# Performance work log

Hardware: AMD Instinct MI355X
Metric: run time of the kernel (lower is better)

The kernel has to match this reference:

```python
import jax, jax.numpy as jnp
import numpy as np

B, T, C = 16, 512, 768
MULT = 4
D_IN = C * MULT          # 3072
HIDDEN = 1024
N_DATES = 16
STACK_SIZE, STACK_STRIDE = 4, 2
MAX_F = 512
N_MASK_TYPES = 5
N_SESSIONS = 4
SCALE = HIDDEN ** 0.5


def setup_inputs() -> dict:
    key = jax.random.key(0)
    ks = jax.random.split(key, 12)
    inp = {
        "spikes": jax.random.normal(ks[0], (B, T, C), dtype=jnp.float32),
        "spikes_mask": jnp.ones((B, T), dtype=jnp.int64),
        "spikes_timestamp": jax.random.randint(ks[1], (B, T), 0, 255).astype(jnp.int64),
        "date_idx": jax.random.randint(ks[2], (B,), 0, N_DATES).astype(jnp.int64),
        "mask_idx": 1,
        "session_idx": 3,
        # params
        "W_embed": jax.random.normal(ks[3], (N_DATES, D_IN, C), dtype=jnp.float32) * 0.02,
        "b_embed": jax.random.normal(ks[4], (N_DATES, D_IN), dtype=jnp.float32) * 0.02,
        "W_stack": jax.random.normal(ks[5], (HIDDEN, D_IN * STACK_SIZE), dtype=jnp.float32) * 0.02,
        "b_stack": jax.random.normal(ks[6], (HIDDEN,), dtype=jnp.float32) * 0.02,
        "pos_table": jax.random.normal(ks[7], (MAX_F, HIDDEN), dtype=jnp.float32) * 0.02,
        "prompt_table": jax.random.normal(ks[8], (N_MASK_TYPES, HIDDEN), dtype=jnp.float32) * 0.02,
        "session_table": jax.random.normal(ks[9], (N_SESSIONS, HIDDEN), dtype=jnp.float32) * 0.02,
    }
    return inp


def reference(spikes, spikes_mask, spikes_timestamp, date_idx, mask_idx, session_idx,
              W_embed, b_embed, W_stack, b_stack, pos_table, prompt_table, session_table):
    Bb = spikes.shape[0]
    # adapt branch: per-sample expert Linear, done as one gather + batched GEMM
    W = W_embed[date_idx]                      # [B, D_IN, C]
    b = b_embed[date_idx]                      # [B, D_IN]
    x = jnp.einsum('btc,bdc->btd', spikes, W) + b[:, None, :]   # [B, T, D_IN]
    x = jax.nn.gelu(x, approximate=False) * SCALE
    # unfold-based stacking: sliding windows over time
    L = (T - STACK_SIZE) // STACK_STRIDE + 1   # 255
    starts = jnp.arange(L) * STACK_STRIDE
    widx = starts[:, None] + jnp.arange(STACK_SIZE)             # [L, size]
    win = x[:, widx, :]                                         # [B, L, size, D_IN]
    stacked = win.reshape(Bb, L, STACK_SIZE * D_IN)
    x = stacked @ W_stack.T + b_stack                           # [B, L, HIDDEN]
    ts = spikes_timestamp[:, :L]
    mask = jnp.prod(spikes_mask[:, widx], axis=-1)              # [B, L]
    # positional embedding
    x = x + pos_table[ts]
    # prompt token
    x = jnp.concatenate(
        [jnp.broadcast_to(prompt_table[mask_idx][None, None, :], (Bb, 1, HIDDEN)), x], axis=1)
    mask = jnp.pad(mask, ((0, 0), (1, 0)), constant_values=1)
    ts = jnp.concatenate([jnp.zeros((Bb, 1), ts.dtype), ts + 1], axis=1)
    # session token
    x = jnp.concatenate(
        [jnp.broadcast_to(session_table[session_idx][None, None, :], (Bb, 1, HIDDEN)), x], axis=1)
    mask = jnp.pad(mask, ((0, 0), (1, 0)), constant_values=1)
    ts = jnp.concatenate([jnp.zeros((Bb, 1), ts.dtype), ts + 1], axis=1)
    # dropout is identity in eval
    return x, mask, ts
```

## Files before the change

### kernel.cpp

```cpp
#include <hip/hip_runtime.h>
#include <hip/hip_bf16.h>

#define BATCH   16
#define TT      512
#define CC      768
#define D_IN    3072
#define HIDDEN  1024
#define LL      255
#define OUTROWS 257
#define KSTACK  12288

typedef float f32x4 __attribute__((ext_vector_type(4)));
typedef __bf16 bf16x8 __attribute__((ext_vector_type(8)));
typedef unsigned short u16;

__device__ __forceinline__ u16 f2bf(float f) {
    unsigned u = __builtin_bit_cast(unsigned, f);
    u = (u + 0x7FFFu + ((u >> 16) & 1u)) >> 16;
    return (u16)u;
}

__device__ __forceinline__ bf16x8 lds_read8(const u16* p) {
    return __builtin_bit_cast(bf16x8, *(const uint4*)p);
}

__device__ __forceinline__ void gload16(const u16* g, u16* l) {
    __builtin_amdgcn_global_load_lds(
        (const __attribute__((address_space(1))) void*)g,
        (__attribute__((address_space(3))) void*)l, 16, 0, 0);
}

__global__ __launch_bounds__(256) void cvt_wstack(const float* __restrict__ W, u16* __restrict__ out) {
    size_t i = ((size_t)blockIdx.x * 256 + threadIdx.x) * 4;
    size_t stride = (size_t)gridDim.x * 256 * 4;
    for (; i < (size_t)HIDDEN * KSTACK; i += stride) {
        float4 v = *(const float4*)(W + i);
        ushort4 o = make_ushort4(f2bf(v.x), f2bf(v.y), f2bf(v.z), f2bf(v.w));
        *(ushort4*)(out + i) = o;
    }
}

__global__ __launch_bounds__(256) void gemm1(const float* __restrict__ spikes,
                                             const float* __restrict__ W_embed,
                                             const float* __restrict__ b_embed,
                                             const int* __restrict__ date_idx,
                                             u16* __restrict__ x1) {
    const int m0 = blockIdx.x * 128;
    const int n0 = blockIdx.y * 128;
    const int bb = blockIdx.z;
    const int date = date_idx[bb];
    const float* A  = spikes  + (size_t)bb  * TT * CC;
    const float* Bw = W_embed + (size_t)date * D_IN * CC;

    __shared__ u16 As[128 * 64];
    __shared__ u16 Bs[128 * 64];

    const int tid  = threadIdx.x;
    const int lane = tid & 63;
    const int wave = tid >> 6;
    const int wm = wave >> 1, wn = wave & 1;

    f32x4 acc[4][4] = {};

    for (int k0 = 0; k0 < CC; k0 += 64) {
        {
            const int c4 = tid & 15;
            int r = tid >> 4;
            #pragma unroll
            for (int p = 0; p < 8; ++p, r += 16) {
                float4 va = *(const float4*)(A  + (size_t)(m0 + r) * CC + k0 + c4 * 4);
                float4 vb = *(const float4*)(Bw + (size_t)(n0 + r) * CC + k0 + c4 * 4);
                const int col = c4 * 4;
                const int idx = r * 64 + (col ^ ((r & 7) << 3));
                *(ushort4*)(&As[idx]) = make_ushort4(f2bf(va.x), f2bf(va.y), f2bf(va.z), f2bf(va.w));
                *(ushort4*)(&Bs[idx]) = make_ushort4(f2bf(vb.x), f2bf(vb.y), f2bf(vb.z), f2bf(vb.w));
            }
        }
        __syncthreads();
        #pragma unroll
        for (int kk = 0; kk < 64; kk += 32) {
            bf16x8 af[4], bfr[4];
            const int krow = lane & 15;
            const int kcol = kk + ((lane >> 4) << 3);
            #pragma unroll
            for (int i = 0; i < 4; ++i) {
                const int ra = wm * 64 + i * 16 + krow;
                af[i]  = lds_read8(&As[ra * 64 + (kcol ^ ((ra & 7) << 3))]);
                const int rb = wn * 64 + i * 16 + krow;
                bfr[i] = lds_read8(&Bs[rb * 64 + (kcol ^ ((rb & 7) << 3))]);
            }
            #pragma unroll
            for (int i = 0; i < 4; ++i)
                #pragma unroll
                for (int j = 0; j < 4; ++j)
                    acc[i][j] = __builtin_amdgcn_mfma_f32_16x16x32_bf16(af[i], bfr[j], acc[i][j], 0, 0, 0);
        }
        __syncthreads();
    }

    const float* be = b_embed + (size_t)date * D_IN;
    #pragma unroll
    for (int i = 0; i < 4; ++i) {
        #pragma unroll
        for (int j = 0; j < 4; ++j) {
            const int col  = n0 + wn * 64 + j * 16 + (lane & 15);
            const float bias = be[col];
            const int rbase = m0 + wm * 64 + i * 16 + ((lane >> 4) << 2);
            #pragma unroll
            for (int q = 0; q < 4; ++q) {
                float v = acc[i][j][q] + bias;
                float g = 0.5f * v * (1.0f + erff(v * 0.70710678118654752f)) * 32.0f;
                x1[(size_t)bb * TT * D_IN + (size_t)(rbase + q) * D_IN + col] = f2bf(g);
            }
        }
    }
}

template <bool WRITE_PART>
__global__ __launch_bounds__(512, 2) void gemm2(const u16* __restrict__ x1,
                                                const u16* __restrict__ Wbf,
                                                float* __restrict__ part,
                                                const float* __restrict__ b_stack,
                                                const float* __restrict__ pos_table,
                                                const int* __restrict__ tstamp,
                                                float* __restrict__ out,
                                                int KS) {
    const int n0 = blockIdx.x * 256;
    const int ks = blockIdx.y;
    const int bb = blockIdx.z;
    const int KCH  = KSTACK / KS;
    const int kbeg = ks * KCH;
    const int nt   = KCH / 64;
    const u16* Xb = x1 + (size_t)bb * TT * D_IN;

    __shared__ u16 Asm[2 * 256 * 64];
    __shared__ u16 Bsm[2 * 256 * 64];

    const int tid  = threadIdx.x;
    const int lane = tid & 63;
    const int wave = tid >> 6;
    const int wm = wave >> 2;
    const int wn = wave & 3;

    const int lrow = lane >> 3;
    const int scol = ((lane & 7) ^ lrow) << 3;

    f32x4 acc[8][4] = {};

    auto STAGE = [&](int k0, int buf) {
        const int s  = k0 / D_IN;
        const int d0 = k0 % D_IN;
        u16* Ad = Asm + buf * (256 * 64);
        u16* Bd = Bsm + buf * (256 * 64);
        #pragma unroll
        for (int i = 0; i < 4; ++i) {
            const int rb = i * 8 + wave;
            const int row = rb * 8 + lrow;
            int gl = row; if (gl > LL - 1) gl = LL - 1;
            gload16(Xb + (size_t)(2 * gl + s) * D_IN + d0 + scol, Ad + rb * 512);
            gload16(Wbf + (size_t)(n0 + row) * KSTACK + k0 + scol, Bd + rb * 512);
        }
    };

    STAGE(kbeg, 0);
    STAGE(kbeg + 64, 1);

    for (int t = 0; t < nt; ++t) {
        const int cur = t & 1;
        if (t + 1 < nt) { asm volatile("s_waitcnt vmcnt(8)" ::: "memory"); }
        else            { asm volatile("s_waitcnt vmcnt(0)" ::: "memory"); }
        __builtin_amdgcn_s_barrier();
        asm volatile("" ::: "memory");

        const u16* Ab = Asm + cur * (256 * 64);
        const u16* Bb = Bsm + cur * (256 * 64);
        #pragma unroll
        for (int kk = 0; kk < 64; kk += 32) {
            bf16x8 af[8], bfr[4];
            const int krow = lane & 15;
            const int kcol = kk + ((lane >> 4) << 3);
            #pragma unroll
            for (int i = 0; i < 8; ++i) {
                const int ra = wm * 128 + i * 16 + krow;
                af[i] = lds_read8(&Ab[ra * 64 + (kcol ^ ((ra & 7) << 3))]);
            }
            #pragma unroll
            for (int j = 0; j < 4; ++j) {
                const int rb2 = wn * 64 + j * 16 + krow;
                bfr[j] = lds_read8(&Bb[rb2 * 64 + (kcol ^ ((rb2 & 7) << 3))]);
            }
            #pragma unroll
            for (int i = 0; i < 8; ++i)
                #pragma unroll
                for (int j = 0; j < 4; ++j)
                    acc[i][j] = __builtin_amdgcn_mfma_f32_16x16x32_bf16(af[i], bfr[j], acc[i][j], 0, 0, 0);
        }

        asm volatile("" ::: "memory");
        __builtin_amdgcn_s_barrier();
        asm volatile("" ::: "memory");
        if (t + 2 < nt) STAGE(kbeg + (t + 2) * 64, cur);
    }

    if (WRITE_PART) {
        float* pt = part + ((size_t)(ks * BATCH + bb) * 256) * HIDDEN;
        #pragma unroll
        for (int i = 0; i < 8; ++i) {
            #pragma unroll
            for (int j = 0; j < 4; ++j) {
                const int col = n0 + wn * 64 + j * 16 + (lane & 15);
                const int rb  = wm * 128 + i * 16 + ((lane >> 4) << 2);
                #pragma unroll
                for (int q = 0; q < 4; ++q)
                    pt[(size_t)(rb + q) * HIDDEN + col] = acc[i][j][q];
            }
        }
    } else {
        #pragma unroll
        for (int i = 0; i < 8; ++i) {
            #pragma unroll
            for (int j = 0; j < 4; ++j) {
                const int col = n0 + wn * 64 + j * 16 + (lane & 15);
                const int lb  = wm * 128 + i * 16 + ((lane >> 4) << 2);
                #pragma unroll
                for (int q = 0; q < 4; ++q) {
                    const int l = lb + q;
                    if (l < LL) {
                        const int tsv = tstamp[bb * TT + l];
                        float v = acc[i][j][q] + b_stack[col] + pos_table[(size_t)tsv * HIDDEN + col];
                        out[(size_t)bb * OUTROWS * HIDDEN + (size_t)(2 + l) * HIDDEN + col] = v;
                    }
                }
            }
        }
    }
}

__global__ __launch_bounds__(256) void reduce_ep(const float* __restrict__ part,
                                                 const float* __restrict__ b_stack,
                                                 const float* __restrict__ pos_table,
                                                 const int* __restrict__ tstamp,
                                                 float* __restrict__ out,
                                                 int KS) {
    const int idx = blockIdx.x * 256 + threadIdx.x;
    const int c4  = idx & (HIDDEN / 4 - 1);
    const int r   = idx >> 8;
    if (r >= BATCH * LL) return;
    const int l  = r % LL;
    const int bb = r / LL;
    float4 v = make_float4(0.f, 0.f, 0.f, 0.f);
    for (int ks = 0; ks < KS; ++ks) {
        float4 p = *(const float4*)(part + ((size_t)(ks * BATCH + bb) * 256 + l) * HIDDEN + c4 * 4);
        v.x += p.x; v.y += p.y; v.z += p.z; v.w += p.w;
    }
    const int tsv = tstamp[bb * TT + l];
    float4 bs = *(const float4*)(b_stack + c4 * 4);
    float4 ps = *(const float4*)(pos_table + (size_t)tsv * HIDDEN + c4 * 4);
    v.x += bs.x + ps.x; v.y += bs.y + ps.y; v.z += bs.z + ps.z; v.w += bs.w + ps.w;
    *(float4*)(out + ((size_t)bb * OUTROWS + 2 + l) * HIDDEN + c4 * 4) = v;
}

__global__ __launch_bounds__(256) void epilogue_misc(const int* __restrict__ smask,
                                                     const int* __restrict__ tstamp,
                                                     const int* __restrict__ mask_idx_p,
                                                     const int* __restrict__ session_idx_p,
                                                     const float* __restrict__ prompt_table,
                                                     const float* __restrict__ session_table,
                                                     float* __restrict__ out) {
    const int bb = blockIdx.x;
    const int tid = threadIdx.x;
    const int mi = mask_idx_p[0];
    const int si = session_idx_p[0];
    float* xb = out + (size_t)bb * OUTROWS * HIDDEN;
    for (int i = tid; i < HIDDEN; i += 256) {
        xb[i]          = session_table[(size_t)si * HIDDEN + i];
        xb[HIDDEN + i] = prompt_table[(size_t)mi * HIDDEN + i];
    }
    float* maskout = out + (size_t)BATCH * OUTROWS * HIDDEN + (size_t)bb * OUTROWS;
    float* tsout   = out + (size_t)BATCH * OUTROWS * HIDDEN + (size_t)BATCH * OUTROWS + (size_t)bb * OUTROWS;
    for (int j = tid; j < OUTROWS; j += 256) {
        if (j == 0)      { maskout[0] = 1.0f; tsout[0] = 0.0f; }
        else if (j == 1) { maskout[1] = 1.0f; tsout[1] = 1.0f; }
        else {
            const int l = j - 2;
            int m = 1;
            #pragma unroll
            for (int s = 0; s < 4; ++s) m *= smask[bb * TT + 2 * l + s];
            maskout[j] = (float)m;
            tsout[j]   = (float)(tstamp[bb * TT + l] + 2);
        }
    }
}

extern "C" void kernel_launch(void* const* d_in, const int* in_sizes, int n_in,
                              void* d_out, int out_size, void* d_ws, size_t ws_size,
                              hipStream_t stream) {
    const float* spikes      = (const float*)d_in[0];
    const int*   spikes_mask = (const int*)d_in[1];
    const int*   tstamp      = (const int*)d_in[2];
    const int*   date_idx    = (const int*)d_in[3];
    const int*   mask_idx    = (const int*)d_in[4];
    const int*   session_idx = (const int*)d_in[5];
    const float* W_embed     = (const float*)d_in[6];
    const float* b_embed     = (const float*)d_in[7];
    const float* W_stack     = (const float*)d_in[8];
    const float* b_stack     = (const float*)d_in[9];
    const float* pos_table   = (const float*)d_in[10];
    const float* prompt_tab  = (const float*)d_in[11];
    const float* session_tab = (const float*)d_in[12];
    float* out = (float*)d_out;

    const size_t X1_B   = (size_t)BATCH * TT * D_IN * 2;
    const size_t WBF_B  = (size_t)HIDDEN * KSTACK * 2;
    const size_t PART_B = (size_t)BATCH * 256 * HIDDEN * 4;
    u16*   x1   = (u16*)d_ws;
    u16*   Wbf  = (u16*)((char*)d_ws + X1_B);
    float* part = (float*)((char*)d_ws + X1_B + WBF_B);

    int KS = 0;
    if      (ws_size >= X1_B + WBF_B + 4 * PART_B) KS = 4;
    else if (ws_size >= X1_B + WBF_B + 3 * PART_B) KS = 3;
    else if (ws_size >= X1_B + WBF_B + 2 * PART_B) KS = 2;
    else if (ws_size >= X1_B + WBF_B + 1 * PART_B) KS = 1;

    cvt_wstack<<<2048, 256, 0, stream>>>(W_stack, Wbf);
    gemm1<<<dim3(TT / 128, D_IN / 128, BATCH), 256, 0, stream>>>(spikes, W_embed, b_embed, date_idx, x1);
    if (KS > 0) {
        gemm2<true><<<dim3(HIDDEN / 256, KS, BATCH), 512, 0, stream>>>(x1, Wbf, part, b_stack, pos_table, tstamp, out, KS);
        reduce_ep<<<(BATCH * LL * (HIDDEN / 4) + 255) / 256, 256, 0, stream>>>(part, b_stack, pos_table, tstamp, out, KS);
    } else {
        gemm2<false><<<dim3(HIDDEN / 256, 1, BATCH), 512, 0, stream>>>(x1, Wbf, part, b_stack, pos_table, tstamp, out, 1);
    }
    epilogue_misc<<<BATCH, 256, 0, stream>>>(spikes_mask, tstamp, mask_idx, session_idx,
                                             prompt_tab, session_tab, out);
}
```

Baseline: 262.8 us.

## Pre-convert gemm1 inputs to bf16 and use larger async-LDS double-buffered tiles

Spikes and only the W_embed experts that are actually referenced (tracked with a per-date flag kernel) are converted to bf16 in workspace. A new gemm1 kernel then streams them with global_load_lds into double-buffered, swizzled 256x256 tiles using 512 threads. The goal is to halve operand bandwidth and remove the in-loop fp32-to-bf16 conversion, and to overlap loads with MFMA. The cost is extra conversion kernels and launches. The split-K partial buffer now shares workspace space with the bf16 staging buffers.

```diff
diff --git a/kernel.cpp b/kernel.cpp
--- a/kernel.cpp
+++ b/kernel.cpp
@@ -9,6 +9,7 @@
 #define LL      255
 #define OUTROWS 257
 #define KSTACK  12288
+#define N_DATES 16
 
 typedef float f32x4 __attribute__((ext_vector_type(4)));
 typedef __bf16 bf16x8 __attribute__((ext_vector_type(8)));
@@ -40,11 +41,137 @@
     }
 }
 
-__global__ __launch_bounds__(256) void gemm1(const float* __restrict__ spikes,
-                                             const float* __restrict__ W_embed,
-                                             const float* __restrict__ b_embed,
-                                             const int* __restrict__ date_idx,
-                                             u16* __restrict__ x1) {
+__global__ __launch_bounds__(256) void cvt_spikes(const float* __restrict__ in, u16* __restrict__ out) {
+    size_t i = ((size_t)blockIdx.x * 256 + threadIdx.x) * 4;
+    size_t stride = (size_t)gridDim.x * 256 * 4;
+    for (; i < (size_t)BATCH * TT * CC; i += stride) {
+        float4 v = *(const float4*)(in + i);
+        ushort4 o = make_ushort4(f2bf(v.x), f2bf(v.y), f2bf(v.z), f2bf(v.w));
+        *(ushort4*)(out + i) = o;
+    }
+}
+
+__global__ __launch_bounds__(64) void date_flags(const int* __restrict__ date_idx, int* __restrict__ flags) {
+    const int tid = threadIdx.x;
+    if (tid < N_DATES) flags[tid] = 0;
+    __syncthreads();
+    if (tid < BATCH) flags[date_idx[tid]] = 1;
+}
+
+__global__ __launch_bounds__(256) void cvt_wembed(const float* __restrict__ W,
+                                                  const int* __restrict__ flags,
+                                                  u16* __restrict__ out) {
+    const int date = blockIdx.y;
+    if (!flags[date]) return;
+    const size_t bofs = (size_t)date * D_IN * CC;
+    const size_t i = bofs + ((size_t)blockIdx.x * 256 + threadIdx.x) * 4;
+    float4 v = *(const float4*)(W + i);
+    ushort4 o = make_ushort4(f2bf(v.x), f2bf(v.y), f2bf(v.z), f2bf(v.w));
+    *(ushort4*)(out + i) = o;
+}
+
+__global__ __launch_bounds__(512, 2) void gemm1_bf(const u16* __restrict__ spk,
+                                                   const u16* __restrict__ wemb,
+                                                   const float* __restrict__ b_embed,
+                                                   const int* __restrict__ date_idx,
+                                                   u16* __restrict__ x1) {
+    const int m0 = blockIdx.x * 256;
+    const int n0 = blockIdx.y * 256;
+    const int bb = blockIdx.z;
+    const int date = date_idx[bb];
+    const u16* A  = spk  + (size_t)bb   * TT * CC;
+    const u16* Bw = wemb + (size_t)date * D_IN * CC;
+    const int nt = CC / 64;
+
+    __shared__ u16 Asm[2 * 256 * 64];
+    __shared__ u16 Bsm[2 * 256 * 64];
+
+    const int tid  = threadIdx.x;
+    const int lane = tid & 63;
+    const int wave = tid >> 6;
+    const int wm = wave >> 2;
+    const int wn = wave & 3;
+
+    const int lrow = lane >> 3;
+    const int scol = ((lane & 7) ^ lrow) << 3;
+
+    f32x4 acc[8][4] = {};
+
+    auto STAGE = [&](int k0, int buf) {
+        u16* Ad = Asm + buf * (256 * 64);
+        u16* Bd = Bsm + buf * (256 * 64);
+        #pragma unroll
+        for (int i = 0; i < 4; ++i) {
+            const int rb = i * 8 + wave;
+            const int row = rb * 8 + lrow;
+            gload16(A  + (size_t)(m0 + row) * CC + k0 + scol, Ad + rb * 512);
+            gload16(Bw + (size_t)(n0 + row) * CC + k0 + scol, Bd + rb * 512);
+        }
+    };
+
+    STAGE(0, 0);
+    STAGE(64, 1);
+
+    for (int t = 0; t < nt; ++t) {
+        const int cur = t & 1;
+        if (t + 1 < nt) { asm volatile("s_waitcnt vmcnt(8)" ::: "memory"); }
+        else            { asm volatile("s_waitcnt vmcnt(0)" ::: "memory"); }
+        __builtin_amdgcn_s_barrier();
+        asm volatile("" ::: "memory");
+
+        const u16* Ab = Asm + cur * (256 * 64);
+        const u16* Bb = Bsm + cur * (256 * 64);
+        #pragma unroll
+        for (int kk = 0; kk < 64; kk += 32) {
+            bf16x8 af[8], bfr[4];
+            const int krow = lane & 15;
+            const int kcol = kk + ((lane >> 4) << 3);
+            #pragma unroll
+            for (int i = 0; i < 8; ++i) {
+                const int ra = wm * 128 + i * 16 + krow;
+                af[i] = lds_read8(&Ab[ra * 64 + (kcol ^ ((ra & 7) << 3))]);
+            }
+            #pragma unroll
+            for (int j = 0; j < 4; ++j) {
+                const int rb2 = wn * 64 + j * 16 + krow;
+                bfr[j] = lds_read8(&Bb[rb2 * 64 + (kcol ^ ((rb2 & 7) << 3))]);
+            }
+            #pragma unroll
+            for (int i = 0; i < 8; ++i)
+                #pragma unroll
+                for (int j = 0; j < 4; ++j)
+                    acc[i][j] = __builtin_amdgcn_mfma_f32_16x16x32_bf16(af[i], bfr[j], acc[i][j], 0, 0, 0);
+        }
+
+        asm volatile("" ::: "memory");
+        __builtin_amdgcn_s_barrier();
+        asm volatile("" ::: "memory");
+        if (t + 2 < nt) STAGE((t + 2) * 64, cur);
+    }
+
+    const float* be = b_embed + (size_t)date * D_IN;
+    #pragma unroll
+    for (int i = 0; i < 8; ++i) {
+        #pragma unroll
+        for (int j = 0; j < 4; ++j) {
+            const int col  = n0 + wn * 64 + j * 16 + (lane & 15);
+            const float bias = be[col];
+            const int rbase = m0 + wm * 128 + i * 16 + ((lane >> 4) << 2);
+            #pragma unroll
+            for (int q = 0; q < 4; ++q) {
+                float v = acc[i][j][q] + bias;
+                float g = 0.5f * v * (1.0f + erff(v * 0.70710678118654752f)) * 32.0f;
+                x1[(size_t)bb * TT * D_IN + (size_t)(rbase + q) * D_IN + col] = f2bf(g);
+            }
+        }
+    }
+}
+
+__global__ __launch_bounds__(256) void gemm1_f32(const float* __restrict__ spikes,
+                                                 const float* __restrict__ W_embed,
+                                                 const float* __restrict__ b_embed,
+                                                 const int* __restrict__ date_idx,
+                                                 u16* __restrict__ x1) {
     const int m0 = blockIdx.x * 128;
     const int n0 = blockIdx.y * 128;
     const int bb = blockIdx.z;
@@ -313,18 +440,38 @@
     const size_t X1_B   = (size_t)BATCH * TT * D_IN * 2;
     const size_t WBF_B  = (size_t)HIDDEN * KSTACK * 2;
     const size_t PART_B = (size_t)BATCH * 256 * HIDDEN * 4;
-    u16*   x1   = (u16*)d_ws;
-    u16*   Wbf  = (u16*)((char*)d_ws + X1_B);
-    float* part = (float*)((char*)d_ws + X1_B + WBF_B);
-
+    const size_t FLAGS_B = 4096;
+    const size_t SPK_B  = (size_t)BATCH * TT * CC * 2;
+    const size_t WEMB_B = (size_t)N_DATES * D_IN * CC * 2;
+    const size_t BASE   = X1_B + WBF_B;
+    const size_t UNION_BF = FLAGS_B + SPK_B + WEMB_B;
+
+    u16*   x1    = (u16*)d_ws;
+    u16*   Wbf   = (u16*)((char*)d_ws + X1_B);
+    int*   flags = (int*)((char*)d_ws + BASE);
+    u16*   spkbf = (u16*)((char*)d_ws + BASE + FLAGS_B);
+    u16*   wembf = (u16*)((char*)d_ws + BASE + FLAGS_B + SPK_B);
+    float* part  = (float*)((char*)d_ws + BASE);
+
+    const bool use_bf = (ws_size >= BASE + UNION_BF);
     int KS = 0;
-    if      (ws_size >= X1_B + WBF_B + 4 * PART_B) KS = 4;
-    else if (ws_size >= X1_B + WBF_B + 3 * PART_B) KS = 3;
-    else if (ws_size >= X1_B + WBF_B + 2 * PART_B) KS = 2;
-    else if (ws_size >= X1_B + WBF_B + 1 * PART_B) KS = 1;
+    if (use_bf) KS = 4;
+    else {
+        size_t rem = (ws_size > BASE) ? (ws_size - BASE) : 0;
+        KS = (int)(rem / PART_B); if (KS > 4) KS = 4;
+    }
 
     cvt_wstack<<<2048, 256, 0, stream>>>(W_stack, Wbf);
-    gemm1<<<dim3(TT / 128, D_IN / 128, BATCH), 256, 0, stream>>>(spikes, W_embed, b_embed, date_idx, x1);
+
+    if (use_bf) {
+        date_flags<<<1, 64, 0, stream>>>(date_idx, flags);
+        cvt_spikes<<<2048, 256, 0, stream>>>(spikes, spkbf);
+        cvt_wembed<<<dim3(D_IN * CC / 4 / 256, N_DATES), 256, 0, stream>>>(W_embed, flags, wembf);
+        gemm1_bf<<<dim3(TT / 256, D_IN / 256, BATCH), 512, 0, stream>>>(spkbf, wembf, b_embed, date_idx, x1);
+    } else {
+        gemm1_f32<<<dim3(TT / 128, D_IN / 128, BATCH), 256, 0, stream>>>(spikes, W_embed, b_embed, date_idx, x1);
+    }
+
     if (KS > 0) {
         gemm2<true><<<dim3(HIDDEN / 256, KS, BATCH), 512, 0, stream>>>(x1, Wbf, part, b_stack, pos_table, tstamp, out, KS);
         reduce_ep<<<(BATCH * LL * (HIDDEN / 4) + 255) / 256, 256, 0, stream>>>(part, b_stack, pos_table, tstamp, out, KS);
```

New measurement: 265.0 us. About the same (+0.8%).
